# Performance work log

Hardware: AMD Instinct MI355X
Metric: run time of the kernel (lower is better)

The kernel has to match this reference:

```python
import jax, jax.numpy as jnp
import numpy as np

N_NODES = 500000
N_EDGES = 8000000


def gcn_conv(x, W, b, src, dst, n_nodes):
    # PyG GCNConv: add self-loops, symmetric normalization, x@W, scatter-add.
    loop = jnp.arange(n_nodes, dtype=src.dtype)
    src_a = jnp.concatenate([src, loop])  # [E+N]
    dst_a = jnp.concatenate([dst, loop])
    deg = jax.ops.segment_sum(jnp.ones_like(dst_a, dtype=x.dtype), dst_a,
                              num_segments=n_nodes)  # in-degree incl. self-loop
    dinv = jnp.where(deg > 0, jax.lax.rsqrt(deg), 0.0)
    norm = dinv[src_a] * dinv[dst_a]  # [E+N]
    xw = x @ W  # [N, out]
    msg = xw[src_a] * norm[:, None]  # [E+N, out]
    out = jax.ops.segment_sum(msg, dst_a, num_segments=n_nodes)
    return out + b


def setup_inputs() -> dict:
    key = jax.random.key(0)
    k1, k2, k3, k4, k5, k6 = jax.random.split(key, 6)
    x = jax.random.uniform(k1, (N_NODES, 1), dtype=jnp.float32)
    edge_index = jax.random.randint(k2, (2, N_EDGES), 0, N_NODES, dtype=jnp.int32)
    W1 = jax.random.normal(k3, (1, 16), dtype=jnp.float32)
    b1 = jax.random.normal(k4, (16,), dtype=jnp.float32) * 0.1
    W2 = jax.random.normal(k5, (16, 2), dtype=jnp.float32)
    b2 = jax.random.normal(k6, (2,), dtype=jnp.float32) * 0.1
    return {"x": x, "edge_index": edge_index, "W1": W1, "b1": b1,
            "W2": W2, "b2": b2}


def reference(x, edge_index, W1, b1, W2, b2):
    src, dst = edge_index[0], edge_index[1]
    h = gcn_conv(x, W1, b1, src, dst, N_NODES)
    h = jax.nn.relu(h)
    # dropout is identity in eval mode
    h = gcn_conv(h, W2, b2, src, dst, N_NODES)
    return jax.nn.log_softmax(h, axis=1)
```

## Files before the change

### kernel.cpp

```cpp
#include <hip/hip_runtime.h>
#include <math.h>


typedef unsigned int uint4v __attribute__((ext_vector_type(4)));

#define NPB 1024
#define NPB_SHIFT 10
#define NPB_MASK (NPB - 1)
#define MAXB 512
#define P1T 512
#define CHUNK 16384
#define P2_THREADS 1024

#define NTL4(p) __builtin_nontemporal_load((const uint4v*)(p))

__device__ __forceinline__ unsigned short f2bf(float f) {
    unsigned int x = __float_as_uint(f);
    x += 0x7fffu + ((x >> 16) & 1u);
    return (unsigned short)(x >> 16);
}
__device__ __forceinline__ float bf2f(unsigned short h) {
    return __uint_as_float((unsigned int)h << 16);
}

__global__ __launch_bounds__(P1T, 4) void k_bucket(
    const int* __restrict__ src, const int* __restrict__ dst,
    unsigned int* __restrict__ file, int* __restrict__ ctr,
    int E, int nbucket, int cap)
{
    __shared__ unsigned int sorted[CHUNK];
    __shared__ int cnt[MAXB];
    __shared__ int pre[MAXB + 1];
    __shared__ int gb[MAXB];
    __shared__ int rk[MAXB];

    const int t  = threadIdx.x;
    const int e0 = blockIdx.x * CHUNK;
    const int nE = min(CHUNK, E - e0);

    for (int b = t; b < MAXB; b += P1T) { cnt[b] = 0; rk[b] = 0; }
    __syncthreads();

    const bool full = (nE == CHUNK);
    int4 dc[8];

    if (full) {
        const int4* d4 = (const int4*)(dst + e0);
#pragma unroll
        for (int k = 0; k < 8; ++k) dc[k] = d4[t + k * P1T];
#pragma unroll
        for (int k = 0; k < 8; ++k) {
            atomicAdd(&cnt[((unsigned)dc[k].x) >> NPB_SHIFT], 1);
            atomicAdd(&cnt[((unsigned)dc[k].y) >> NPB_SHIFT], 1);
            atomicAdd(&cnt[((unsigned)dc[k].z) >> NPB_SHIFT], 1);
            atomicAdd(&cnt[((unsigned)dc[k].w) >> NPB_SHIFT], 1);
        }
    } else {
        for (int i = t; i < nE; i += P1T)
            atomicAdd(&cnt[((unsigned)dst[e0 + i]) >> NPB_SHIFT], 1);
    }
    __syncthreads();

    int v = (t < nbucket) ? cnt[t] : 0;
    pre[t + 1] = v;
    if (t == 0) pre[0] = 0;
    __syncthreads();
    for (int off = 1; off < P1T; off <<= 1) {
        int add = (t >= off) ? pre[t + 1 - off] : 0;
        __syncthreads();
        pre[t + 1] += add;
        __syncthreads();
    }

    for (int b = t; b < nbucket; b += P1T) {
        int c = cnt[b];
        gb[b] = c ? atomicAdd(&ctr[b], c) : 0;
    }
    __syncthreads();

    if (full) {
        const int4* s4 = (const int4*)(src + e0);
#pragma unroll
        for (int k = 0; k < 8; ++k) {
            int4 s = s4[t + k * P1T];
            int4 d = dc[k];
            {
                int b = ((unsigned)d.x) >> NPB_SHIFT;
                int r = atomicAdd(&rk[b], 1);
                sorted[pre[b] + r] = (((unsigned)s.x) << NPB_SHIFT) | ((unsigned)d.x & NPB_MASK);
            }
            {
                int b = ((unsigned)d.y) >> NPB_SHIFT;
                int r = atomicAdd(&rk[b], 1);
                sorted[pre[b] + r] = (((unsigned)s.y) << NPB_SHIFT) | ((unsigned)d.y & NPB_MASK);
            }
            {
                int b = ((unsigned)d.z) >> NPB_SHIFT;
                int r = atomicAdd(&rk[b], 1);
                sorted[pre[b] + r] = (((unsigned)s.z) << NPB_SHIFT) | ((unsigned)d.z & NPB_MASK);
            }
            {
                int b = ((unsigned)d.w) >> NPB_SHIFT;
                int r = atomicAdd(&rk[b], 1);
                sorted[pre[b] + r] = (((unsigned)s.w) << NPB_SHIFT) | ((unsigned)d.w & NPB_MASK);
            }
        }
    } else {
        for (int i = t; i < nE; i += P1T) {
            int d = dst[e0 + i];
            int b = ((unsigned)d) >> NPB_SHIFT;
            unsigned int w = (((unsigned)src[e0 + i]) << NPB_SHIFT) |
                             ((unsigned)d & NPB_MASK);
            int r = atomicAdd(&rk[b], 1);
            sorted[pre[b] + r] = w;
        }
    }
    __syncthreads();

    {
        const int wid  = t >> 6;
        const int lane = t & 63;
        const int nw   = P1T >> 6;
        for (int b = wid; b < nbucket; b += nw) {
            int s0 = pre[b], s1 = pre[b + 1];
            unsigned int* dp = file + (size_t)b * cap + gb[b];
            for (int j = s0 + lane; j < s1; j += 64)
                __builtin_nontemporal_store(sorted[j], &dp[j - s0]);
        }
    }
}

__global__ __launch_bounds__(P2_THREADS, 8) void k_deg_node1(
    const unsigned int* __restrict__ file, const int* __restrict__ ctr,
    const float* __restrict__ x, float* __restrict__ dinv,
    unsigned short* __restrict__ u, int N, int cap)
{
    __shared__ int cnt[NPB];
    const int b = blockIdx.x;
    cnt[threadIdx.x] = 0;
    __syncthreads();
    const int n = ctr[b];
    const unsigned int* f = file + (size_t)b * cap;
    const int T4 = P2_THREADS * 4;
    int i = threadIdx.x * 4;
    for (; i + T4 + 3 < n; i += 2 * T4) {
        uint4v w0 = NTL4(f + i);
        uint4v w1 = NTL4(f + i + T4);
        atomicAdd(&cnt[w0.x & NPB_MASK], 1);
        atomicAdd(&cnt[w0.y & NPB_MASK], 1);
        atomicAdd(&cnt[w0.z & NPB_MASK], 1);
        atomicAdd(&cnt[w0.w & NPB_MASK], 1);
        atomicAdd(&cnt[w1.x & NPB_MASK], 1);
        atomicAdd(&cnt[w1.y & NPB_MASK], 1);
        atomicAdd(&cnt[w1.z & NPB_MASK], 1);
        atomicAdd(&cnt[w1.w & NPB_MASK], 1);
    }
    for (; i + 3 < n; i += T4) {
        uint4v w = NTL4(f + i);
        atomicAdd(&cnt[w.x & NPB_MASK], 1);
        atomicAdd(&cnt[w.y & NPB_MASK], 1);
        atomicAdd(&cnt[w.z & NPB_MASK], 1);
        atomicAdd(&cnt[w.w & NPB_MASK], 1);
    }
    for (int j = (n & ~3) + threadIdx.x; j < n; j += P2_THREADS)
        atomicAdd(&cnt[__builtin_nontemporal_load(f + j) & NPB_MASK], 1);
    __syncthreads();
    const int g = b * NPB + threadIdx.x;
    if (g < N) {
        float dv = rsqrtf((float)(cnt[threadIdx.x] + 1));
        dinv[g] = dv;
        u[g] = f2bf(x[g] * dv);
    }
}

__global__ __launch_bounds__(P2_THREADS, 8) void k_agg1_mlp(
    const unsigned int* __restrict__ file, const int* __restrict__ ctr,
    const unsigned short* __restrict__ u, const float* __restrict__ dinv,
    const float* __restrict__ W1, const float* __restrict__ b1,
    const float* __restrict__ W2, unsigned int* __restrict__ q, int N, int cap)
{
    __shared__ float acc[NPB];
    const int b = blockIdx.x;
    acc[threadIdx.x] = 0.f;
    __syncthreads();
    const int n = ctr[b];
    const unsigned int* f = file + (size_t)b * cap;
    const int T4 = P2_THREADS * 4;
    int i = threadIdx.x * 4;
    for (; i + T4 + 3 < n; i += 2 * T4) {
        uint4v w0 = NTL4(f + i);
        uint4v w1 = NTL4(f + i + T4);
        float v0 = bf2f(u[w0.x >> NPB_SHIFT]);
        float v1 = bf2f(u[w0.y >> NPB_SHIFT]);
        float v2 = bf2f(u[w0.z >> NPB_SHIFT]);
        float v3 = bf2f(u[w0.w >> NPB_SHIFT]);
        float v4 = bf2f(u[w1.x >> NPB_SHIFT]);
        float v5 = bf2f(u[w1.y >> NPB_SHIFT]);
        float v6 = bf2f(u[w1.z >> NPB_SHIFT]);
        float v7 = bf2f(u[w1.w >> NPB_SHIFT]);
        atomicAdd(&acc[w0.x & NPB_MASK], v0);
        atomicAdd(&acc[w0.y & NPB_MASK], v1);
        atomicAdd(&acc[w0.z & NPB_MASK], v2);
        atomicAdd(&acc[w0.w & NPB_MASK], v3);
        atomicAdd(&acc[w1.x & NPB_MASK], v4);
        atomicAdd(&acc[w1.y & NPB_MASK], v5);
        atomicAdd(&acc[w1.z & NPB_MASK], v6);
        atomicAdd(&acc[w1.w & NPB_MASK], v7);
    }
    for (; i + 3 < n; i += T4) {
        uint4v w = NTL4(f + i);
        float v0 = bf2f(u[w.x >> NPB_SHIFT]);
        float v1 = bf2f(u[w.y >> NPB_SHIFT]);
        float v2 = bf2f(u[w.z >> NPB_SHIFT]);
        float v3 = bf2f(u[w.w >> NPB_SHIFT]);
        atomicAdd(&acc[w.x & NPB_MASK], v0);
        atomicAdd(&acc[w.y & NPB_MASK], v1);
        atomicAdd(&acc[w.z & NPB_MASK], v2);
        atomicAdd(&acc[w.w & NPB_MASK], v3);
    }
    for (int j = (n & ~3) + threadIdx.x; j < n; j += P2_THREADS) {
        unsigned int w = __builtin_nontemporal_load(f + j);
        atomicAdd(&acc[w & NPB_MASK], bf2f(u[w >> NPB_SHIFT]));
    }
    __syncthreads();
    const int g = b * NPB + threadIdx.x;
    if (g < N) {
        float dv = dinv[g];
        float s1 = (acc[threadIdx.x] + bf2f(u[g])) * dv;
        float c0 = 0.f, c1 = 0.f;
#pragma unroll
        for (int k = 0; k < 16; ++k) {
            float h = fmaxf(fmaf(s1, W1[k], b1[k]), 0.f);
            c0 = fmaf(h, W2[2 * k], c0);
            c1 = fmaf(h, W2[2 * k + 1], c1);
        }
        q[g] = (unsigned int)f2bf(c0 * dv) |
               ((unsigned int)f2bf(c1 * dv) << 16);
    }
}

__global__ __launch_bounds__(P2_THREADS, 8) void k_agg2_out(
    const unsigned int* __restrict__ file, const int* __restrict__ ctr,
    const unsigned int* __restrict__ q, const float* __restrict__ dinv,
    const float* __restrict__ b2, float2* __restrict__ out, int N, int cap)
{
    __shared__ float a0[NPB];
    __shared__ float a1[NPB];
    const int b = blockIdx.x;
    a0[threadIdx.x] = 0.f;
    a1[threadIdx.x] = 0.f;
    __syncthreads();
    const int n = ctr[b];
    const unsigned int* f = file + (size_t)b * cap;
    const int T4 = P2_THREADS * 4;
    int i = threadIdx.x * 4;
    for (; i + T4 + 3 < n; i += 2 * T4) {
        uint4v w0 = NTL4(f + i);
        uint4v w1 = NTL4(f + i + T4);
        unsigned int g0 = q[w0.x >> NPB_SHIFT];
        unsigned int g1 = q[w0.y >> NPB_SHIFT];
        unsigned int g2 = q[w0.z >> NPB_SHIFT];
        unsigned int g3 = q[w0.w >> NPB_SHIFT];
        unsigned int g4 = q[w1.x >> NPB_SHIFT];
        unsigned int g5 = q[w1.y >> NPB_SHIFT];
        unsigned int g6 = q[w1.z >> NPB_SHIFT];
        unsigned int g7 = q[w1.w >> NPB_SHIFT];
        atomicAdd(&a0[w0.x & NPB_MASK], bf2f((unsigned short)g0));
        atomicAdd(&a1[w0.x & NPB_MASK], bf2f((unsigned short)(g0 >> 16)));
        atomicAdd(&a0[w0.y & NPB_MASK], bf2f((unsigned short)g1));
        atomicAdd(&a1[w0.y & NPB_MASK], bf2f((unsigned short)(g1 >> 16)));
        atomicAdd(&a0[w0.z & NPB_MASK], bf2f((unsigned short)g2));
        atomicAdd(&a1[w0.z & NPB_MASK], bf2f((unsigned short)(g2 >> 16)));
        atomicAdd(&a0[w0.w & NPB_MASK], bf2f((unsigned short)g3));
        atomicAdd(&a1[w0.w & NPB_MASK], bf2f((unsigned short)(g3 >> 16)));
        atomicAdd(&a0[w1.x & NPB_MASK], bf2f((unsigned short)g4));
        atomicAdd(&a1[w1.x & NPB_MASK], bf2f((unsigned short)(g4 >> 16)));
        atomicAdd(&a0[w1.y & NPB_MASK], bf2f((unsigned short)g5));
        atomicAdd(&a1[w1.y & NPB_MASK], bf2f((unsigned short)(g5 >> 16)));
        atomicAdd(&a0[w1.z & NPB_MASK], bf2f((unsigned short)g6));
        atomicAdd(&a1[w1.z & NPB_MASK], bf2f((unsigned short)(g6 >> 16)));
        atomicAdd(&a0[w1.w & NPB_MASK], bf2f((unsigned short)g7));
        atomicAdd(&a1[w1.w & NPB_MASK], bf2f((unsigned short)(g7 >> 16)));
    }
    for (; i + 3 < n; i += T4) {
        uint4v w = NTL4(f + i);
        unsigned int g0 = q[w.x >> NPB_SHIFT];
        unsigned int g1 = q[w.y >> NPB_SHIFT];
        unsigned int g2 = q[w.z >> NPB_SHIFT];
        unsigned int g3 = q[w.w >> NPB_SHIFT];
        atomicAdd(&a0[w.x & NPB_MASK], bf2f((unsigned short)g0));
        atomicAdd(&a1[w.x & NPB_MASK], bf2f((unsigned short)(g0 >> 16)));
        atomicAdd(&a0[w.y & NPB_MASK], bf2f((unsigned short)g1));
        atomicAdd(&a1[w.y & NPB_MASK], bf2f((unsigned short)(g1 >> 16)));
        atomicAdd(&a0[w.z & NPB_MASK], bf2f((unsigned short)g2));
        atomicAdd(&a1[w.z & NPB_MASK], bf2f((unsigned short)(g2 >> 16)));
        atomicAdd(&a0[w.w & NPB_MASK], bf2f((unsigned short)g3));
        atomicAdd(&a1[w.w & NPB_MASK], bf2f((unsigned short)(g3 >> 16)));
    }
    for (int j = (n & ~3) + threadIdx.x; j < n; j += P2_THREADS) {
        unsigned int w = __builtin_nontemporal_load(f + j);
        unsigned int gq = q[w >> NPB_SHIFT];
        atomicAdd(&a0[w & NPB_MASK], bf2f((unsigned short)gq));
        atomicAdd(&a1[w & NPB_MASK], bf2f((unsigned short)(gq >> 16)));
    }
    __syncthreads();
    const int g = b * NPB + threadIdx.x;
    if (g < N) {
        float dv = dinv[g];
        unsigned int qi = q[g];
        float o0 = (a0[threadIdx.x] + bf2f((unsigned short)qi)) * dv + b2[0];
        float o1 = (a1[threadIdx.x] + bf2f((unsigned short)(qi >> 16))) * dv + b2[1];
        float m = fmaxf(o0, o1);
        float l = m + logf(expf(o0 - m) + expf(o1 - m));
        out[g] = make_float2(o0 - l, o1 - l);
    }
}

#define NT 256
__global__ __launch_bounds__(NT) void fb_deg(const int* __restrict__ dst,
                                             int* __restrict__ deg, int E) {
    int e = blockIdx.x * blockDim.x + threadIdx.x;
    if (e < E) atomicAdd(&deg[dst[e]], 1);
}
__global__ __launch_bounds__(NT) void fb_node1(const float* __restrict__ x,
                                               const int* __restrict__ deg,
                                               float* __restrict__ dinv,
                                               float* __restrict__ u, int N) {
    int i = blockIdx.x * blockDim.x + threadIdx.x;
    if (i < N) {
        float dv = rsqrtf((float)(deg[i] + 1));
        dinv[i] = dv;
        u[i] = x[i] * dv;
    }
}
__global__ __launch_bounds__(NT) void fb_edge1(const int* __restrict__ src,
                                               const int* __restrict__ dst,
                                               const float* __restrict__ u,
                                               float* __restrict__ agg1, int E) {
    int e = blockIdx.x * blockDim.x + threadIdx.x;
    if (e < E) atomicAdd(&agg1[dst[e]], u[src[e]]);
}
__global__ __launch_bounds__(NT) void fb_node2(const float* __restrict__ agg1,
                                               const float* __restrict__ u,
                                               const float* __restrict__ dinv,
                                               const float* __restrict__ W1,
                                               const float* __restrict__ b1,
                                               const float* __restrict__ W2,
                                               float2* __restrict__ q, int N) {
    int i = blockIdx.x * blockDim.x + threadIdx.x;
    if (i < N) {
        float dv = dinv[i];
        float s1 = (agg1[i] + u[i]) * dv;
        float c0 = 0.f, c1 = 0.f;
#pragma unroll
        for (int k = 0; k < 16; ++k) {
            float h = fmaxf(fmaf(s1, W1[k], b1[k]), 0.f);
            c0 = fmaf(h, W2[2 * k], c0);
            c1 = fmaf(h, W2[2 * k + 1], c1);
        }
        q[i] = make_float2(c0 * dv, c1 * dv);
    }
}
__global__ __launch_bounds__(NT) void fb_edge2(const int* __restrict__ src,
                                               const int* __restrict__ dst,
                                               const float2* __restrict__ q,
                                               float* __restrict__ agg2, int E) {
    int e = blockIdx.x * blockDim.x + threadIdx.x;
    if (e < E) {
        float2 qq = q[src[e]];
        atomicAdd(&agg2[2 * dst[e]], qq.x);
        atomicAdd(&agg2[2 * dst[e] + 1], qq.y);
    }
}
__global__ __launch_bounds__(NT) void fb_node3(const float* __restrict__ agg2,
                                               const float2* __restrict__ q,
                                               const float* __restrict__ dinv,
                                               const float* __restrict__ b2,
                                               float2* __restrict__ out, int N) {
    int i = blockIdx.x * blockDim.x + threadIdx.x;
    if (i < N) {
        float dv = dinv[i];
        float2 qi = q[i];
        float o0 = (agg2[2 * i] + qi.x) * dv + b2[0];
        float o1 = (agg2[2 * i + 1] + qi.y) * dv + b2[1];
        float m = fmaxf(o0, o1);
        float l = m + logf(expf(o0 - m) + expf(o1 - m));
        out[i] = make_float2(o0 - l, o1 - l);
    }
}

extern "C" void kernel_launch(void* const* d_in, const int* in_sizes, int n_in,
                              void* d_out, int out_size, void* d_ws, size_t ws_size,
                              hipStream_t stream) {
    const float* x  = (const float*)d_in[0];
    const int* ei   = (const int*)d_in[1];
    const float* W1 = (const float*)d_in[2];
    const float* b1 = (const float*)d_in[3];
    const float* W2 = (const float*)d_in[4];
    const float* b2 = (const float*)d_in[5];

    const int N = in_sizes[0];
    const int E = in_sizes[1] / 2;
    const int* src = ei;
    const int* dst = ei + E;

    const int nbucket = (N + NPB - 1) / NPB;
    const int cap = ((E / nbucket + 4096) + 63) & ~63;

    auto align_up = [](size_t v) { return (v + 255) & ~(size_t)255; };
    size_t off_ctr  = 0;
    size_t off_file = align_up((size_t)MAXB * sizeof(int));
    size_t off_dinv = align_up(off_file + (size_t)nbucket * cap * sizeof(unsigned int));
    size_t off_u    = align_up(off_dinv + (size_t)N * sizeof(float));
    size_t off_q    = align_up(off_u + (size_t)N * sizeof(unsigned short));
    size_t needed   = off_q + (size_t)N * sizeof(unsigned int);

    char* ws = (char*)d_ws;

    if (nbucket <= MAXB && needed <= ws_size) {
        int*            ctr  = (int*)(ws + off_ctr);
        unsigned int*   file = (unsigned int*)(ws + off_file);
        float*          dinv = (float*)(ws + off_dinv);
        unsigned short* u    = (unsigned short*)(ws + off_u);
        unsigned int*   q    = (unsigned int*)(ws + off_q);

        (void)hipMemsetAsync(ctr, 0, (size_t)MAXB * sizeof(int), stream);

        const int p1Blocks = (E + CHUNK - 1) / CHUNK;
        k_bucket   <<<p1Blocks, P1T, 0, stream>>>(src, dst, file, ctr, E, nbucket, cap);
        k_deg_node1<<<nbucket, P2_THREADS, 0, stream>>>(file, ctr, x, dinv, u, N, cap);
        k_agg1_mlp <<<nbucket, P2_THREADS, 0, stream>>>(file, ctr, u, dinv, W1, b1, W2, q, N, cap);
        k_agg2_out <<<nbucket, P2_THREADS, 0, stream>>>(file, ctr, q, dinv, b2, (float2*)d_out, N, cap);
    } else {
        int*    deg  = (int*)   (ws);
        float*  agg1 = (float*) (ws + (size_t)4 * N);
        float*  agg2 = (float*) (ws + (size_t)8 * N);
        float*  dinv = (float*) (ws + (size_t)16 * N);
        float*  u    = (float*) (ws + (size_t)20 * N);
        float2* q    = (float2*)(ws + (size_t)24 * N);
        (void)hipMemsetAsync(ws, 0, (size_t)16 * N, stream);
        const int nodeBlocks = (N + NT - 1) / NT;
        const int edgeBlocks = (E + NT - 1) / NT;
        fb_deg  <<<edgeBlocks, NT, 0, stream>>>(dst, deg, E);
        fb_node1<<<nodeBlocks, NT, 0, stream>>>(x, deg, dinv, u, N);
        fb_edge1<<<edgeBlocks, NT, 0, stream>>>(src, dst, u, agg1, E);
        fb_node2<<<nodeBlocks, NT, 0, stream>>>(agg1, u, dinv, W1, b1, W2, q, N);
        fb_edge2<<<edgeBlocks, NT, 0, stream>>>(src, dst, q, agg2, E);
        fb_node3<<<nodeBlocks, NT, 0, stream>>>(agg2, q, dinv, b2, (float2*)d_out, N);
    }
}
```

Baseline: 279.8 us.

## Sort bucketed edges into per-node CSR and aggregate per node without atomics

A new per-bucket sort kernel counts edges per destination node in LDS, prefix-sums the counts, and rewrites each bucket so edges are grouped by destination. It also stores per-node start offsets. The two aggregation kernels become thread-per-node gathers that sum neighbour values in registers, replacing the LDS float atomics. In exchange the edge file gets an extra read and write pass. The bucket store also silently drops edges beyond a fixed capacity, so a bucket that overflows would lose edges.

```diff
diff --git a/kernel.cpp b/kernel.cpp
--- a/kernel.cpp
+++ b/kernel.cpp
@@ -10,9 +10,8 @@
 #define MAXB 512
 #define P1T 512
 #define CHUNK 16384
-#define P2_THREADS 1024
-
-#define NTL4(p) __builtin_nontemporal_load((const uint4v*)(p))
+#define SORT_CAP 17408
+#define SPT 17
 
 __device__ __forceinline__ unsigned short f2bf(float f) {
     unsigned int x = __float_as_uint(f);
@@ -123,197 +122,153 @@
         const int nw   = P1T >> 6;
         for (int b = wid; b < nbucket; b += nw) {
             int s0 = pre[b], s1 = pre[b + 1];
-            unsigned int* dp = file + (size_t)b * cap + gb[b];
-            for (int j = s0 + lane; j < s1; j += 64)
-                __builtin_nontemporal_store(sorted[j], &dp[j - s0]);
+            int base = gb[b];
+            unsigned int* dp = file + (size_t)b * cap;
+            for (int j = s0 + lane; j < s1; j += 64) {
+                int idx = base + (j - s0);
+                if (idx < cap)
+                    __builtin_nontemporal_store(sorted[j], &dp[idx]);
+            }
         }
     }
 }
 
-__global__ __launch_bounds__(P2_THREADS, 8) void k_deg_node1(
-    const unsigned int* __restrict__ file, const int* __restrict__ ctr,
-    const float* __restrict__ x, float* __restrict__ dinv,
-    unsigned short* __restrict__ u, int N, int cap)
+__global__ __launch_bounds__(NPB) void k_sort(
+    unsigned int* __restrict__ file, const int* __restrict__ ctr,
+    int* __restrict__ start, const float* __restrict__ x,
+    float* __restrict__ dinv, unsigned short* __restrict__ u,
+    int N, int cap)
 {
+    __shared__ unsigned int sorted[SORT_CAP];
     __shared__ int cnt[NPB];
+    __shared__ int pre[NPB + 1];
+
+    const int t = threadIdx.x;
     const int b = blockIdx.x;
-    cnt[threadIdx.x] = 0;
-    __syncthreads();
-    const int n = ctr[b];
-    const unsigned int* f = file + (size_t)b * cap;
-    const int T4 = P2_THREADS * 4;
-    int i = threadIdx.x * 4;
-    for (; i + T4 + 3 < n; i += 2 * T4) {
-        uint4v w0 = NTL4(f + i);
-        uint4v w1 = NTL4(f + i + T4);
-        atomicAdd(&cnt[w0.x & NPB_MASK], 1);
-        atomicAdd(&cnt[w0.y & NPB_MASK], 1);
-        atomicAdd(&cnt[w0.z & NPB_MASK], 1);
-        atomicAdd(&cnt[w0.w & NPB_MASK], 1);
-        atomicAdd(&cnt[w1.x & NPB_MASK], 1);
-        atomicAdd(&cnt[w1.y & NPB_MASK], 1);
-        atomicAdd(&cnt[w1.z & NPB_MASK], 1);
-        atomicAdd(&cnt[w1.w & NPB_MASK], 1);
-    }
-    for (; i + 3 < n; i += T4) {
-        uint4v w = NTL4(f + i);
-        atomicAdd(&cnt[w.x & NPB_MASK], 1);
-        atomicAdd(&cnt[w.y & NPB_MASK], 1);
-        atomicAdd(&cnt[w.z & NPB_MASK], 1);
-        atomicAdd(&cnt[w.w & NPB_MASK], 1);
-    }
-    for (int j = (n & ~3) + threadIdx.x; j < n; j += P2_THREADS)
-        atomicAdd(&cnt[__builtin_nontemporal_load(f + j) & NPB_MASK], 1);
-    __syncthreads();
-    const int g = b * NPB + threadIdx.x;
+    const int nb = min(ctr[b], cap);
+    unsigned int* f = file + (size_t)b * cap;
+
+    cnt[t] = 0;
+    __syncthreads();
+
+    unsigned int ev[SPT];
+    int rk_[SPT];
+#pragma unroll
+    for (int k = 0; k < SPT; ++k) {
+        int i = t + (k << NPB_SHIFT);
+        if (i < nb) ev[k] = __builtin_nontemporal_load(f + i);
+    }
+#pragma unroll
+    for (int k = 0; k < SPT; ++k) {
+        int i = t + (k << NPB_SHIFT);
+        if (i < nb) rk_[k] = atomicAdd(&cnt[ev[k] & NPB_MASK], 1);
+    }
+    __syncthreads();
+
+    pre[t + 1] = cnt[t];
+    if (t == 0) pre[0] = 0;
+    __syncthreads();
+    for (int off = 1; off < NPB; off <<= 1) {
+        int add = (t >= off) ? pre[t + 1 - off] : 0;
+        __syncthreads();
+        pre[t + 1] += add;
+        __syncthreads();
+    }
+
+#pragma unroll
+    for (int k = 0; k < SPT; ++k) {
+        int i = t + (k << NPB_SHIFT);
+        if (i < nb)
+            sorted[pre[ev[k] & NPB_MASK] + rk_[k]] = ev[k] >> NPB_SHIFT;
+    }
+    __syncthreads();
+
+    for (int i = t; i < nb; i += NPB)
+        __builtin_nontemporal_store(sorted[i], &f[i]);
+
+    start[b * (NPB + 1) + t] = pre[t];
+    if (t == 0) start[b * (NPB + 1) + NPB] = pre[NPB];
+
+    const int g = b * NPB + t;
     if (g < N) {
-        float dv = rsqrtf((float)(cnt[threadIdx.x] + 1));
+        float dv = rsqrtf((float)(cnt[t] + 1));
         dinv[g] = dv;
         u[g] = f2bf(x[g] * dv);
     }
 }
 
-__global__ __launch_bounds__(P2_THREADS, 8) void k_agg1_mlp(
-    const unsigned int* __restrict__ file, const int* __restrict__ ctr,
+__global__ __launch_bounds__(256) void k_agg1(
+    const unsigned int* __restrict__ file, const int* __restrict__ start,
     const unsigned short* __restrict__ u, const float* __restrict__ dinv,
     const float* __restrict__ W1, const float* __restrict__ b1,
-    const float* __restrict__ W2, unsigned int* __restrict__ q, int N, int cap)
+    const float* __restrict__ W2, unsigned int* __restrict__ q,
+    int N, int cap)
 {
-    __shared__ float acc[NPB];
-    const int b = blockIdx.x;
-    acc[threadIdx.x] = 0.f;
-    __syncthreads();
-    const int n = ctr[b];
+    int g = blockIdx.x * 256 + threadIdx.x;
+    if (g >= N) return;
+    int b = g >> NPB_SHIFT, loc = g & NPB_MASK;
+    const int* st = start + b * (NPB + 1);
+    int e0 = st[loc], e1 = st[loc + 1];
     const unsigned int* f = file + (size_t)b * cap;
-    const int T4 = P2_THREADS * 4;
-    int i = threadIdx.x * 4;
-    for (; i + T4 + 3 < n; i += 2 * T4) {
-        uint4v w0 = NTL4(f + i);
-        uint4v w1 = NTL4(f + i + T4);
-        float v0 = bf2f(u[w0.x >> NPB_SHIFT]);
-        float v1 = bf2f(u[w0.y >> NPB_SHIFT]);
-        float v2 = bf2f(u[w0.z >> NPB_SHIFT]);
-        float v3 = bf2f(u[w0.w >> NPB_SHIFT]);
-        float v4 = bf2f(u[w1.x >> NPB_SHIFT]);
-        float v5 = bf2f(u[w1.y >> NPB_SHIFT]);
-        float v6 = bf2f(u[w1.z >> NPB_SHIFT]);
-        float v7 = bf2f(u[w1.w >> NPB_SHIFT]);
-        atomicAdd(&acc[w0.x & NPB_MASK], v0);
-        atomicAdd(&acc[w0.y & NPB_MASK], v1);
-        atomicAdd(&acc[w0.z & NPB_MASK], v2);
-        atomicAdd(&acc[w0.w & NPB_MASK], v3);
-        atomicAdd(&acc[w1.x & NPB_MASK], v4);
-        atomicAdd(&acc[w1.y & NPB_MASK], v5);
-        atomicAdd(&acc[w1.z & NPB_MASK], v6);
-        atomicAdd(&acc[w1.w & NPB_MASK], v7);
-    }
-    for (; i + 3 < n; i += T4) {
-        uint4v w = NTL4(f + i);
-        float v0 = bf2f(u[w.x >> NPB_SHIFT]);
-        float v1 = bf2f(u[w.y >> NPB_SHIFT]);
-        float v2 = bf2f(u[w.z >> NPB_SHIFT]);
-        float v3 = bf2f(u[w.w >> NPB_SHIFT]);
-        atomicAdd(&acc[w.x & NPB_MASK], v0);
-        atomicAdd(&acc[w.y & NPB_MASK], v1);
-        atomicAdd(&acc[w.z & NPB_MASK], v2);
-        atomicAdd(&acc[w.w & NPB_MASK], v3);
-    }
-    for (int j = (n & ~3) + threadIdx.x; j < n; j += P2_THREADS) {
-        unsigned int w = __builtin_nontemporal_load(f + j);
-        atomicAdd(&acc[w & NPB_MASK], bf2f(u[w >> NPB_SHIFT]));
-    }
-    __syncthreads();
-    const int g = b * NPB + threadIdx.x;
-    if (g < N) {
-        float dv = dinv[g];
-        float s1 = (acc[threadIdx.x] + bf2f(u[g])) * dv;
-        float c0 = 0.f, c1 = 0.f;
-#pragma unroll
-        for (int k = 0; k < 16; ++k) {
-            float h = fmaxf(fmaf(s1, W1[k], b1[k]), 0.f);
-            c0 = fmaf(h, W2[2 * k], c0);
-            c1 = fmaf(h, W2[2 * k + 1], c1);
-        }
-        q[g] = (unsigned int)f2bf(c0 * dv) |
-               ((unsigned int)f2bf(c1 * dv) << 16);
-    }
-}
-
-__global__ __launch_bounds__(P2_THREADS, 8) void k_agg2_out(
-    const unsigned int* __restrict__ file, const int* __restrict__ ctr,
+
+    float acc = 0.f;
+    int j = e0;
+    for (; j + 4 <= e1; j += 4) {
+        unsigned int s0 = f[j], s1 = f[j + 1], s2 = f[j + 2], s3 = f[j + 3];
+        float a = bf2f(u[s0]), bb = bf2f(u[s1]);
+        float c = bf2f(u[s2]), d = bf2f(u[s3]);
+        acc += (a + bb) + (c + d);
+    }
+    for (; j < e1; ++j) acc += bf2f(u[f[j]]);
+
+    float dv = dinv[g];
+    float s1v = (acc + bf2f(u[g])) * dv;
+    float c0 = 0.f, c1 = 0.f;
+#pragma unroll
+    for (int k = 0; k < 16; ++k) {
+        float h = fmaxf(fmaf(s1v, W1[k], b1[k]), 0.f);
+        c0 = fmaf(h, W2[2 * k], c0);
+        c1 = fmaf(h, W2[2 * k + 1], c1);
+    }
+    q[g] = (unsigned int)f2bf(c0 * dv) | ((unsigned int)f2bf(c1 * dv) << 16);
+}
+
+__global__ __launch_bounds__(256) void k_agg2(
+    const unsigned int* __restrict__ file, const int* __restrict__ start,
     const unsigned int* __restrict__ q, const float* __restrict__ dinv,
-    const float* __restrict__ b2, float2* __restrict__ out, int N, int cap)
+    const float* __restrict__ b2, float2* __restrict__ out,
+    int N, int cap)
 {
-    __shared__ float a0[NPB];
-    __shared__ float a1[NPB];
-    const int b = blockIdx.x;
-    a0[threadIdx.x] = 0.f;
-    a1[threadIdx.x] = 0.f;
-    __syncthreads();
-    const int n = ctr[b];
+    int g = blockIdx.x * 256 + threadIdx.x;
+    if (g >= N) return;
+    int b = g >> NPB_SHIFT, loc = g & NPB_MASK;
+    const int* st = start + b * (NPB + 1);
+    int e0 = st[loc], e1 = st[loc + 1];
     const unsigned int* f = file + (size_t)b * cap;
-    const int T4 = P2_THREADS * 4;
-    int i = threadIdx.x * 4;
-    for (; i + T4 + 3 < n; i += 2 * T4) {
-        uint4v w0 = NTL4(f + i);
-        uint4v w1 = NTL4(f + i + T4);
-        unsigned int g0 = q[w0.x >> NPB_SHIFT];
-        unsigned int g1 = q[w0.y >> NPB_SHIFT];
-        unsigned int g2 = q[w0.z >> NPB_SHIFT];
-        unsigned int g3 = q[w0.w >> NPB_SHIFT];
-        unsigned int g4 = q[w1.x >> NPB_SHIFT];
-        unsigned int g5 = q[w1.y >> NPB_SHIFT];
-        unsigned int g6 = q[w1.z >> NPB_SHIFT];
-        unsigned int g7 = q[w1.w >> NPB_SHIFT];
-        atomicAdd(&a0[w0.x & NPB_MASK], bf2f((unsigned short)g0));
-        atomicAdd(&a1[w0.x & NPB_MASK], bf2f((unsigned short)(g0 >> 16)));
-        atomicAdd(&a0[w0.y & NPB_MASK], bf2f((unsigned short)g1));
-        atomicAdd(&a1[w0.y & NPB_MASK], bf2f((unsigned short)(g1 >> 16)));
-        atomicAdd(&a0[w0.z & NPB_MASK], bf2f((unsigned short)g2));
-        atomicAdd(&a1[w0.z & NPB_MASK], bf2f((unsigned short)(g2 >> 16)));
-        atomicAdd(&a0[w0.w & NPB_MASK], bf2f((unsigned short)g3));
-        atomicAdd(&a1[w0.w & NPB_MASK], bf2f((unsigned short)(g3 >> 16)));
-        atomicAdd(&a0[w1.x & NPB_MASK], bf2f((unsigned short)g4));
-        atomicAdd(&a1[w1.x & NPB_MASK], bf2f((unsigned short)(g4 >> 16)));
-        atomicAdd(&a0[w1.y & NPB_MASK], bf2f((unsigned short)g5));
-        atomicAdd(&a1[w1.y & NPB_MASK], bf2f((unsigned short)(g5 >> 16)));
-        atomicAdd(&a0[w1.z & NPB_MASK], bf2f((unsigned short)g6));
-        atomicAdd(&a1[w1.z & NPB_MASK], bf2f((unsigned short)(g6 >> 16)));
-        atomicAdd(&a0[w1.w & NPB_MASK], bf2f((unsigned short)g7));
-        atomicAdd(&a1[w1.w & NPB_MASK], bf2f((unsigned short)(g7 >> 16)));
-    }
-    for (; i + 3 < n; i += T4) {
-        uint4v w = NTL4(f + i);
-        unsigned int g0 = q[w.x >> NPB_SHIFT];
-        unsigned int g1 = q[w.y >> NPB_SHIFT];
-        unsigned int g2 = q[w.z >> NPB_SHIFT];
-        unsigned int g3 = q[w.w >> NPB_SHIFT];
-        atomicAdd(&a0[w.x & NPB_MASK], bf2f((unsigned short)g0));
-        atomicAdd(&a1[w.x & NPB_MASK], bf2f((unsigned short)(g0 >> 16)));
-        atomicAdd(&a0[w.y & NPB_MASK], bf2f((unsigned short)g1));
-        atomicAdd(&a1[w.y & NPB_MASK], bf2f((unsigned short)(g1 >> 16)));
-        atomicAdd(&a0[w.z & NPB_MASK], bf2f((unsigned short)g2));
-        atomicAdd(&a1[w.z & NPB_MASK], bf2f((unsigned short)(g2 >> 16)));
-        atomicAdd(&a0[w.w & NPB_MASK], bf2f((unsigned short)g3));
-        atomicAdd(&a1[w.w & NPB_MASK], bf2f((unsigned short)(g3 >> 16)));
-    }
-    for (int j = (n & ~3) + threadIdx.x; j < n; j += P2_THREADS) {
-        unsigned int w = __builtin_nontemporal_load(f + j);
-        unsigned int gq = q[w >> NPB_SHIFT];
-        atomicAdd(&a0[w & NPB_MASK], bf2f((unsigned short)gq));
-        atomicAdd(&a1[w & NPB_MASK], bf2f((unsigned short)(gq >> 16)));
-    }
-    __syncthreads();
-    const int g = b * NPB + threadIdx.x;
-    if (g < N) {
-        float dv = dinv[g];
-        unsigned int qi = q[g];
-        float o0 = (a0[threadIdx.x] + bf2f((unsigned short)qi)) * dv + b2[0];
-        float o1 = (a1[threadIdx.x] + bf2f((unsigned short)(qi >> 16))) * dv + b2[1];
-        float m = fmaxf(o0, o1);
-        float l = m + logf(expf(o0 - m) + expf(o1 - m));
-        out[g] = make_float2(o0 - l, o1 - l);
-    }
+
+    float a0 = 0.f, a1 = 0.f;
+    int j = e0;
+    for (; j + 4 <= e1; j += 4) {
+        unsigned int g0 = q[f[j]], g1 = q[f[j + 1]];
+        unsigned int g2 = q[f[j + 2]], g3 = q[f[j + 3]];
+        a0 += (bf2f((unsigned short)g0) + bf2f((unsigned short)g1)) +
+              (bf2f((unsigned short)g2) + bf2f((unsigned short)g3));
+        a1 += (bf2f((unsigned short)(g0 >> 16)) + bf2f((unsigned short)(g1 >> 16))) +
+              (bf2f((unsigned short)(g2 >> 16)) + bf2f((unsigned short)(g3 >> 16)));
+    }
+    for (; j < e1; ++j) {
+        unsigned int gq = q[f[j]];
+        a0 += bf2f((unsigned short)gq);
+        a1 += bf2f((unsigned short)(gq >> 16));
+    }
+
+    float dv = dinv[g];
+    unsigned int qi = q[g];
+    float o0 = (a0 + bf2f((unsigned short)qi)) * dv + b2[0];
+    float o1 = (a1 + bf2f((unsigned short)(qi >> 16))) * dv + b2[1];
+    float m = fmaxf(o0, o1);
+    float l = m + logf(expf(o0 - m) + expf(o1 - m));
+    out[g] = make_float2(o0 - l, o1 - l);
 }
 
 #define NT 256
@@ -405,32 +360,35 @@
     const int* dst = ei + E;
 
     const int nbucket = (N + NPB - 1) / NPB;
-    const int cap = ((E / nbucket + 4096) + 63) & ~63;
+    const int cap = ((E / nbucket + 1024) + 63) & ~63;
 
     auto align_up = [](size_t v) { return (v + 255) & ~(size_t)255; };
-    size_t off_ctr  = 0;
-    size_t off_file = align_up((size_t)MAXB * sizeof(int));
-    size_t off_dinv = align_up(off_file + (size_t)nbucket * cap * sizeof(unsigned int));
-    size_t off_u    = align_up(off_dinv + (size_t)N * sizeof(float));
-    size_t off_q    = align_up(off_u + (size_t)N * sizeof(unsigned short));
-    size_t needed   = off_q + (size_t)N * sizeof(unsigned int);
+    size_t off_ctr   = 0;
+    size_t off_file  = align_up((size_t)MAXB * sizeof(int));
+    size_t off_start = align_up(off_file + (size_t)nbucket * SORT_CAP * sizeof(unsigned int));
+    size_t off_dinv  = align_up(off_start + (size_t)nbucket * (NPB + 1) * sizeof(int));
+    size_t off_u     = align_up(off_dinv + (size_t)N * sizeof(float));
+    size_t off_q     = align_up(off_u + (size_t)N * sizeof(unsigned short));
+    size_t needed    = off_q + (size_t)N * sizeof(unsigned int);
 
     char* ws = (char*)d_ws;
 
-    if (nbucket <= MAXB && needed <= ws_size) {
-        int*            ctr  = (int*)(ws + off_ctr);
-        unsigned int*   file = (unsigned int*)(ws + off_file);
-        float*          dinv = (float*)(ws + off_dinv);
-        unsigned short* u    = (unsigned short*)(ws + off_u);
-        unsigned int*   q    = (unsigned int*)(ws + off_q);
+    if (nbucket <= MAXB && cap <= SORT_CAP && needed <= ws_size) {
+        int*            ctr   = (int*)(ws + off_ctr);
+        unsigned int*   file  = (unsigned int*)(ws + off_file);
+        int*            start = (int*)(ws + off_start);
+        float*          dinv  = (float*)(ws + off_dinv);
+        unsigned short* u     = (unsigned short*)(ws + off_u);
+        unsigned int*   q     = (unsigned int*)(ws + off_q);
 
         (void)hipMemsetAsync(ctr, 0, (size_t)MAXB * sizeof(int), stream);
 
-        const int p1Blocks = (E + CHUNK - 1) / CHUNK;
-        k_bucket   <<<p1Blocks, P1T, 0, stream>>>(src, dst, file, ctr, E, nbucket, cap);
-        k_deg_node1<<<nbucket, P2_THREADS, 0, stream>>>(file, ctr, x, dinv, u, N, cap);
-        k_agg1_mlp <<<nbucket, P2_THREADS, 0, stream>>>(file, ctr, u, dinv, W1, b1, W2, q, N, cap);
-        k_agg2_out <<<nbucket, P2_THREADS, 0, stream>>>(file, ctr, q, dinv, b2, (float2*)d_out, N, cap);
+        const int p1Blocks  = (E + CHUNK - 1) / CHUNK;
+        const int nodBlocks = (N + 255) / 256;
+        k_bucket<<<p1Blocks, P1T, 0, stream>>>(src, dst, file, ctr, E, nbucket, SORT_CAP);
+        k_sort  <<<nbucket, NPB, 0, stream>>>(file, ctr, start, x, dinv, u, N, SORT_CAP);
+        k_agg1  <<<nodBlocks, 256, 0, stream>>>(file, start, u, dinv, W1, b1, W2, q, N, SORT_CAP);
+        k_agg2  <<<nodBlocks, 256, 0, stream>>>(file, start, q, dinv, b2, (float2*)d_out, N, SORT_CAP);
     } else {
         int*    deg  = (int*)   (ws);
         float*  agg1 = (float*) (ws + (size_t)4 * N);
```

After: 237.8 us. 1.18x faster.
